# Optimization experiments

Hardware: AMD Instinct MI355X
Metric: run time of the kernel (lower is better)

## Reference

```python
import jax, jax.numpy as jnp
import numpy as np

N_HEADS = 16

def _rotate_half(t):
    # t: [B, H, T, hs]; split last dim in half, return cat(-x2, x1)
    hs = t.shape[-1]
    x1, x2 = t[..., : hs // 2], t[..., hs // 2 :]
    return jnp.concatenate((-x2, x1), axis=-1)

def _rope_pos(T, hs, dtype):
    inv_freq = 1.0 / (10000.0 ** (jnp.arange(0, hs, 2, dtype=jnp.float32) / hs))
    freqs = jnp.arange(T, dtype=jnp.float32)[:, None] * inv_freq[None, :]  # [T, hs/2]
    pos = jnp.concatenate((freqs, freqs), axis=-1)  # [T, hs]
    return pos

def setup_inputs() -> dict:
    key = jax.random.key(0)
    ks = jax.random.split(key, 5)
    d = 2048
    x = jax.random.normal(ks[0], (2, 2048, d), dtype=jnp.float32)
    W_attn = jax.random.normal(ks[1], (d, 3 * d), dtype=jnp.float32) * (1.0 / np.sqrt(d))
    b_attn = jax.random.normal(ks[2], (3 * d,), dtype=jnp.float32) * 0.02
    W_proj = jax.random.normal(ks[3], (d, d), dtype=jnp.float32) * (1.0 / np.sqrt(d))
    b_proj = jax.random.normal(ks[4], (d,), dtype=jnp.float32) * 0.02
    return {"x": x, "W_attn": W_attn, "b_attn": b_attn, "W_proj": W_proj, "b_proj": b_proj}

def reference(x, W_attn, b_attn, W_proj, b_proj):
    B, T, C = x.shape
    nh = N_HEADS
    hs = C // nh
    qkv = x @ W_attn + b_attn  # [B, T, 3C]
    q, k, v = jnp.split(qkv, 3, axis=-1)
    # [B, T, C] -> [B, nh, T, hs]
    def to_heads(t):
        return t.reshape(B, T, nh, hs).transpose(0, 2, 1, 3)
    q, k, v = to_heads(q), to_heads(k), to_heads(v)
    # RoPE
    pos = _rope_pos(T, hs, x.dtype)  # [T, hs]
    cos, sin = jnp.cos(pos).astype(x.dtype), jnp.sin(pos).astype(x.dtype)
    q = q * cos + _rotate_half(q) * sin
    k = k * cos + _rotate_half(k) * sin
    # causal SDPA
    scale = 1.0 / np.sqrt(hs)
    scores = jnp.einsum('bhqd,bhkd->bhqk', q, k) * scale  # [B, nh, T, T]
    causal = jnp.tril(jnp.ones((T, T), dtype=bool))
    scores = jnp.where(causal, scores, jnp.finfo(scores.dtype).min)
    att = jax.nn.softmax(scores, axis=-1)
    out = jnp.einsum('bhqk,bhkd->bhqd', att, v)  # [B, nh, T, hs]
    y = out.transpose(0, 2, 1, 3).reshape(B, T, C)
    return y @ W_proj + b_proj
```

## Files before the change

kernel.cpp:

```cpp
#include <hip/hip_runtime.h>
#include <stdint.h>

typedef unsigned short u16;
typedef __attribute__((ext_vector_type(8))) short short8;
typedef __attribute__((ext_vector_type(4))) float f32x4;
typedef __attribute__((ext_vector_type(4))) unsigned short u16x4;

#define DEV __device__ __forceinline__

DEV u16 f2bf(float f) {
  union { float f; unsigned u; } v; v.f = f;
  unsigned r = v.u + 0x7fffu + ((v.u >> 16) & 1u);
  return (u16)(r >> 16);
}
DEV float bf2f(u16 b) {
  union { unsigned u; float f; } v; v.u = ((unsigned)b) << 16;
  return v.f;
}
DEV void gload_lds16(const void* g, void* l) {
  __builtin_amdgcn_global_load_lds((const __attribute__((address_space(1))) void*)g,
                                   (__attribute__((address_space(3))) void*)l,
                                   16, 0, 0);
}
DEV void block_barrier() {
  asm volatile("" ::: "memory");
  __builtin_amdgcn_s_barrier();
  asm volatile("" ::: "memory");
}

__global__ void k_conv(const float* __restrict__ in, u16* __restrict__ out, int n4) {
  int i = blockIdx.x * blockDim.x + threadIdx.x;
  if (i >= n4) return;
  const f32x4 v = *(const f32x4*)(in + (size_t)i * 4);
  u16x4 o;
  o[0] = f2bf(v[0]); o[1] = f2bf(v[1]); o[2] = f2bf(v[2]); o[3] = f2bf(v[3]);
  *(u16x4*)(out + (size_t)i * 4) = o;
}

__global__ void k_tconv(const float* __restrict__ in, u16* __restrict__ out, int R, int C) {
  __shared__ float tile[32][33];
  int c0 = blockIdx.x * 32, r0 = blockIdx.y * 32;
  int tx = threadIdx.x, ty = threadIdx.y;
#pragma unroll
  for (int j = 0; j < 32; j += 8)
    tile[ty + j][tx] = in[(size_t)(r0 + ty + j) * C + (c0 + tx)];
  __syncthreads();
#pragma unroll
  for (int j = 0; j < 32; j += 8)
    out[(size_t)(c0 + ty + j) * R + (r0 + tx)] = f2bf(tile[tx][ty + j]);
}

__global__ void k_rope(const u16* __restrict__ qkv, u16* __restrict__ qh, u16* __restrict__ kh) {
  int m = blockIdx.x;
  int t = m & 2047, b = m >> 11;
  int tid = threadIdx.x;
  int h = blockIdx.y * 4 + (tid >> 6);
  int j = tid & 63;
  float inv = expf((float)j * -0.14391156831212787f);
  float ang = (float)t * inv;
  float s, c;
  sincosf(ang, &s, &c);
  size_t ibase = (size_t)m * 6144 + (size_t)h * 128;
  size_t obase = ((size_t)(b * 16 + h) * 2048 + t) * 128;
  float q1 = bf2f(qkv[ibase + j]),        q2 = bf2f(qkv[ibase + 64 + j]);
  qh[obase + j]      = f2bf(q1 * c - q2 * s);
  qh[obase + 64 + j] = f2bf(q2 * c + q1 * s);
  float k1 = bf2f(qkv[ibase + 2048 + j]), k2 = bf2f(qkv[ibase + 2048 + 64 + j]);
  kh[obase + j]      = f2bf(k1 * c - k2 * s);
  kh[obase + 64 + j] = f2bf(k2 * c + k1 * s);
}

__global__ void k_vtrans(const u16* __restrict__ qkv, u16* __restrict__ vt) {
  __shared__ u16 tile[32][33];
  int bh = blockIdx.z;
  int b = bh >> 4, h = bh & 15;
  int t0 = blockIdx.x * 32, d0 = blockIdx.y * 32;
  int tx = threadIdx.x, ty = threadIdx.y;
#pragma unroll
  for (int j = 0; j < 32; j += 8)
    tile[ty + j][tx] = qkv[(size_t)(b * 2048 + t0 + ty + j) * 6144 + 4096 + h * 128 + d0 + tx];
  __syncthreads();
#pragma unroll
  for (int j = 0; j < 32; j += 8)
    vt[((size_t)bh * 128 + d0 + ty + j) * 2048 + (t0 + tx)] = tile[tx][ty + j];
}

template <bool OUT_BF16, bool SPLITK>
__global__ __launch_bounds__(512, 2) void k_gemm3(const u16* __restrict__ A,
                                                  const u16* __restrict__ Bt,
                                                  const float* __restrict__ bias,
                                                  void* __restrict__ Cv,
                                                  int M, int N, int Kld, int nkt) {
  __shared__ __align__(16) short lA[2][256 * 64];
  __shared__ __align__(16) short lB[2][256 * 64];
  const int tid = threadIdx.x;
  const int wid = tid >> 6, lane = tid & 63;
  const int gx = gridDim.x;
  const int nwg = gx * gridDim.y;
  const int orig = blockIdx.y * gx + blockIdx.x;
  const int lg = (orig & 7) * (nwg >> 3) + (orig >> 3);
  const int bm = (lg % gx) * 256, bn = (lg / gx) * 256;
  const int wr = wid >> 2, wc = wid & 3;
  const int r = lane & 15, kq = lane >> 4, r7 = lane & 7;
  const int kz = SPLITK ? blockIdx.z * (nkt << 6) : 0;

  int aoff[4], boff[4], lbase[4];
#pragma unroll
  for (int j = 0; j < 4; ++j) {
    int c = j * 512 + wid * 64 + lane;
    int row = c >> 3, ch = c & 7;
    aoff[j] = (bm + row) * Kld + kz + (ch ^ (row & 7)) * 8;
    boff[j] = (bn + row) * Kld + kz + (ch ^ (row & 7)) * 8;
    lbase[j] = (j * 512 + wid * 64) * 16;
  }

#define STG_A(k0, buf, j) gload_lds16(A + aoff[j] + (k0), (char*)&lA[(buf)][0] + lbase[j])
#define STG_B(k0, buf, j) gload_lds16(Bt + boff[j] + (k0), (char*)&lB[(buf)][0] + lbase[j])
#define RD_A(AF, MH, KK)                                                        \
  _Pragma("unroll")                                                             \
  for (int m2 = 0; m2 < 4; ++m2)                                                \
    AF[m2] = *(const short8*)&As[(wr * 128 + (MH) * 64 + m2 * 16 + r) * 64      \
                                 + (((KK) * 4 + kq) ^ r7) * 8];
#define RD_B(KK)                                                                \
  _Pragma("unroll")                                                             \
  for (int nf = 0; nf < 4; ++nf)                                                \
    bfr[KK][nf] = *(const short8*)&Bs[(wc * 64 + nf * 16 + r) * 64              \
                                      + (((KK) * 4 + kq) ^ r7) * 8];
#define PH_MFMA(AF, MH, KK)                                                     \
  __builtin_amdgcn_s_setprio(1);                                                \
  _Pragma("unroll")                                                             \
  for (int m2 = 0; m2 < 4; ++m2)                                                \
    _Pragma("unroll")                                                           \
    for (int nf = 0; nf < 4; ++nf)                                              \
      acc[(MH) * 4 + m2][nf] = __builtin_amdgcn_mfma_f32_16x16x32_bf16(         \
          AF[m2], bfr[KK][nf], acc[(MH) * 4 + m2][nf], 0, 0, 0);                \
  __builtin_amdgcn_s_setprio(0);

  f32x4 acc[8][4];
  const f32x4 zero = {0.f, 0.f, 0.f, 0.f};
#pragma unroll
  for (int i = 0; i < 8; ++i)
#pragma unroll
    for (int j = 0; j < 4; ++j) acc[i][j] = zero;

  const int nt = nkt;

#pragma unroll
  for (int j = 0; j < 4; ++j) STG_A(0, 0, j);
#pragma unroll
  for (int j = 0; j < 4; ++j) STG_B(0, 0, j);
  if (nt > 1) {
#pragma unroll
    for (int j = 0; j < 4; ++j) STG_B(64, 1, j);
    asm volatile("s_waitcnt vmcnt(4)" ::: "memory");
  } else {
    asm volatile("s_waitcnt vmcnt(0)" ::: "memory");
  }
  block_barrier();

#pragma unroll 1
  for (int t = 0; t < nt; ++t) {
    const int cur = t & 1, nxt = cur ^ 1;
    const short* As = &lA[cur][0];
    const short* Bs = &lB[cur][0];
    const int kA = (t + 1) * 64, kB = (t + 2) * 64;
    const bool sA = (t + 1 < nt), sB = (t + 2 < nt);
    short8 bfr[2][4];
    short8 af[4];

    RD_B(0)
    RD_A(af, 0, 0)
    if (sA) { STG_A(kA, nxt, 0); STG_A(kA, nxt, 1); }
    block_barrier();
    PH_MFMA(af, 0, 0)
    block_barrier();

    RD_B(1)
    RD_A(af, 0, 1)
    if (sA) { STG_A(kA, nxt, 2); STG_A(kA, nxt, 3); }
    block_barrier();
    PH_MFMA(af, 0, 1)
    block_barrier();

    RD_A(af, 1, 0)
    if (sB) { STG_B(kB, cur, 0); STG_B(kB, cur, 1); }
    block_barrier();
    PH_MFMA(af, 1, 0)
    block_barrier();

    RD_A(af, 1, 1)
    if (sB) { STG_B(kB, cur, 2); STG_B(kB, cur, 3); }
    block_barrier();
    PH_MFMA(af, 1, 1)
    if (t + 1 < nt) {
      if (sB) asm volatile("s_waitcnt vmcnt(4)" ::: "memory");
      else    asm volatile("s_waitcnt vmcnt(0)" ::: "memory");
    }
    block_barrier();
  }
#undef STG_A
#undef STG_B
#undef RD_A
#undef RD_B
#undef PH_MFMA

#pragma unroll
  for (int mf = 0; mf < 8; ++mf)
#pragma unroll
    for (int nf = 0; nf < 4; ++nf) {
      int n = bn + wc * 64 + nf * 16 + r;
      float bv = SPLITK ? 0.f : bias[n];
#pragma unroll
      for (int i = 0; i < 4; ++i) {
        int m = bm + wr * 128 + mf * 16 + kq * 4 + i;
        float val = acc[mf][nf][i] + bv;
        if (SPLITK)
          ((float*)Cv)[(size_t)blockIdx.z * M * N + (size_t)m * N + n] = val;
        else if (OUT_BF16)
          ((u16*)Cv)[(size_t)m * N + n] = f2bf(val);
        else
          ((float*)Cv)[(size_t)m * N + n] = val;
      }
    }
}

__global__ void k_fadd(const float* __restrict__ p, const float* __restrict__ bias,
                       float* __restrict__ y, int n4) {
  const int half4 = 2097152;
  for (int i = blockIdx.x * blockDim.x + threadIdx.x; i < n4; i += gridDim.x * blockDim.x) {
    f32x4 a = *(const f32x4*)(p + (size_t)i * 4);
    f32x4 b = *(const f32x4*)(p + (size_t)(i + half4) * 4);
    f32x4 bv = *(const f32x4*)(bias + ((i & 511) << 2));
    f32x4 o = a + b + bv;
    *(f32x4*)(y + (size_t)i * 4) = o;
  }
}

__global__ __launch_bounds__(256) void k_attn(const u16* __restrict__ qh,
                                              const u16* __restrict__ kh,
                                              const u16* __restrict__ vt,
                                              u16* __restrict__ out) {
  __shared__ __align__(16) short lK[2][64 * 128];
  __shared__ __align__(16) short lV[2][128 * 64];
  __shared__ __align__(16) short lP[64 * 64];
  const int tid = threadIdx.x, wid = tid >> 6, lane = tid & 63;
  const int p = blockIdx.x, h = blockIdx.y, b = blockIdx.z;
  const size_t bh = (size_t)b * 16 + h;
  const u16* qb = qh + bh * 2048 * 128;
  const u16* kb = kh + bh * 2048 * 128;
  const u16* vb = vt + bh * 128 * 2048;
  const int r = lane & 15, kq = lane >> 4;
  const int r7 = r & 7;
  const int wrow = wid * 16;
  const float scale2 = 0.08838834764831845f * 1.4426950408889634f;

  int koff[4], voff[4];
#pragma unroll
  for (int i = 0; i < 4; ++i) {
    int ci = (wid * 4 + i) * 64 + lane;
    int krow = ci >> 4, kch = ci & 15;
    koff[i] = krow * 128 + ((kch ^ (krow & 7)) * 8);
    int vrow = ci >> 3, vch = ci & 7;
    voff[i] = vrow * 2048 + ((vch ^ (vrow & 7)) * 8);
  }

#pragma unroll 1
  for (int seg = 0; seg < 2; ++seg) {
    const int j = seg ? 31 - p : p;
    const int q0 = j * 64;
    const int nkt = j + 1;

    short8 qa[4];
#pragma unroll
    for (int kk = 0; kk < 4; ++kk)
      qa[kk] = *(const short8*)(qb + (size_t)(q0 + wrow + r) * 128 + kk * 32 + kq * 8);

    f32x4 O[8];
    const f32x4 zero = {0.f, 0.f, 0.f, 0.f};
#pragma unroll
    for (int nf = 0; nf < 8; ++nf) O[nf] = zero;
    float lp[4] = {0.f, 0.f, 0.f, 0.f};

#pragma unroll
    for (int i = 0; i < 4; ++i) {
      gload_lds16(kb + koff[i], (char*)&lK[0][0] + (wid * 4 + i) * 1024);
      gload_lds16(vb + voff[i], (char*)&lV[0][0] + (wid * 4 + i) * 1024);
    }

#pragma unroll 1
    for (int kt = 0; kt < nkt; ++kt) {
      const int cur = kt & 1;
      if (kt + 1 < nkt) {
        const size_t kbase = (size_t)(kt + 1) * 8192, vbase = (size_t)(kt + 1) * 64;
#pragma unroll
        for (int i = 0; i < 4; ++i) {
          gload_lds16(kb + kbase + koff[i], (char*)&lK[cur ^ 1][0] + (wid * 4 + i) * 1024);
          gload_lds16(vb + vbase + voff[i], (char*)&lV[cur ^ 1][0] + (wid * 4 + i) * 1024);
        }
        asm volatile("s_waitcnt vmcnt(8)" ::: "memory");
      } else {
        asm volatile("s_waitcnt vmcnt(0)" ::: "memory");
      }
      block_barrier();

      f32x4 S[4];
#pragma unroll
      for (int nf = 0; nf < 4; ++nf) S[nf] = zero;
#pragma unroll
      for (int kk = 0; kk < 4; ++kk) {
        short8 kf[4];
#pragma unroll
        for (int nf = 0; nf < 4; ++nf)
          kf[nf] = *(const short8*)&lK[cur][(nf * 16 + r) * 128 + ((kk * 4 + kq) ^ r7) * 8];
#pragma unroll
        for (int nf = 0; nf < 4; ++nf)
          S[nf] = __builtin_amdgcn_mfma_f32_16x16x32_bf16(qa[kk], kf[nf], S[nf], 0, 0, 0);
      }

      const bool diag = (kt == nkt - 1);
#pragma unroll
      for (int nf = 0; nf < 4; ++nf)
#pragma unroll
        for (int i = 0; i < 4; ++i) {
          float pv = exp2f(S[nf][i] * scale2);
          if (diag) {
            int kg = kt * 64 + nf * 16 + r;
            int qg = q0 + wrow + kq * 4 + i;
            pv = (kg > qg) ? 0.f : pv;
          }
          lp[i] += pv;
          int row = wrow + kq * 4 + i;
          int cl = (nf * 2 + (r >> 3)) ^ ((kq * 4 + i) & 7);
          lP[row * 64 + cl * 8 + r7] = (short)f2bf(pv);
        }

#pragma unroll
      for (int kk = 0; kk < 2; ++kk) {
        short8 pa = *(const short8*)&lP[(wrow + r) * 64 + ((kk * 4 + kq) ^ r7) * 8];
#pragma unroll
        for (int nf = 0; nf < 8; ++nf) {
          short8 vf = *(const short8*)&lV[cur][(nf * 16 + r) * 64 + ((kk * 4 + kq) ^ r7) * 8];
          O[nf] = __builtin_amdgcn_mfma_f32_16x16x32_bf16(pa, vf, O[nf], 0, 0, 0);
        }
      }
      asm volatile("s_waitcnt lgkmcnt(0)" ::: "memory");
      block_barrier();
    }

    float inv[4];
#pragma unroll
    for (int i = 0; i < 4; ++i) {
      float v = lp[i];
      v += __shfl_xor(v, 1);
      v += __shfl_xor(v, 2);
      v += __shfl_xor(v, 4);
      v += __shfl_xor(v, 8);
      inv[i] = 1.f / v;
    }
#pragma unroll
    for (int nf = 0; nf < 8; ++nf)
#pragma unroll
      for (int i = 0; i < 4; ++i) {
        int qg = q0 + wrow + kq * 4 + i;
        out[(size_t)(b * 2048 + qg) * 2048 + h * 128 + nf * 16 + r] = f2bf(O[nf][i] * inv[i]);
      }
  }
}

extern "C" void kernel_launch(void* const* d_in, const int* in_sizes, int n_in,
                              void* d_out, int out_size, void* d_ws, size_t ws_size,
                              hipStream_t stream) {
  const float* x      = (const float*)d_in[0];
  const float* W_attn = (const float*)d_in[1];
  const float* b_attn = (const float*)d_in[2];
  const float* W_proj = (const float*)d_in[3];
  const float* b_proj = (const float*)d_in[4];
  float* y = (float*)d_out;

  u16* xb     = (u16*)d_ws;
  u16* wqkvT  = xb     + (size_t)4096 * 2048;
  u16* wprojT = wqkvT  + (size_t)6144 * 2048;
  u16* qkv    = wprojT + (size_t)2048 * 2048;
  u16* qh     = qkv    + (size_t)4096 * 6144;
  u16* kh     = qh     + (size_t)4096 * 2048;
  u16* vt     = kh     + (size_t)4096 * 2048;
  u16* attout = vt     + (size_t)4096 * 2048;
  if (ws_size < (size_t)83886080 * 2) return;

  float* pproj = (float*)qkv;

  k_conv<<<8192, 256, 0, stream>>>(x, xb, 2097152);
  k_tconv<<<dim3(192, 64), dim3(32, 8), 0, stream>>>(W_attn, wqkvT, 2048, 6144);
  k_tconv<<<dim3(64, 64), dim3(32, 8), 0, stream>>>(W_proj, wprojT, 2048, 2048);
  k_gemm3<true, false><<<dim3(16, 24), 512, 0, stream>>>(xb, wqkvT, b_attn, qkv, 4096, 6144, 2048, 32);
  k_rope<<<dim3(4096, 4), 256, 0, stream>>>(qkv, qh, kh);
  k_vtrans<<<dim3(64, 4, 32), dim3(32, 8), 0, stream>>>(qkv, vt);
  k_attn<<<dim3(16, 16, 2), 256, 0, stream>>>(qh, kh, vt, attout);
  k_gemm3<false, true><<<dim3(16, 8, 2), 512, 0, stream>>>(attout, wprojT, b_proj, pproj, 4096, 2048, 2048, 16);
  k_fadd<<<2048, 256, 0, stream>>>(pproj, b_proj, y, 2097152);
}
```

Baseline: 314.7 us.

## Fuse RoPE and V transpose into QKV GEMM epilogue

Adds a dedicated QKV GEMM whose epilogue applies bias and RoPE and writes Q and K directly in head-major layout. It also writes V transposed, so the separate rope and vtrans kernels and the qkv intermediate are gone. Partner half-dimension values for the rotation are exchanged through LDS, and the angle is advanced with a recurrence after one sincos per fragment. This removes two launches and the round trip of the qkv buffer through global memory. In exchange the epilogue has scattered stores and extra barriers, and the sincos recurrence adds a little numeric drift.

```diff
diff --git a/kernel.cpp b/kernel.cpp
--- a/kernel.cpp
+++ b/kernel.cpp
@@ -50,47 +50,13 @@
     out[(size_t)(c0 + ty + j) * R + (r0 + tx)] = f2bf(tile[tx][ty + j]);
 }
 
-__global__ void k_rope(const u16* __restrict__ qkv, u16* __restrict__ qh, u16* __restrict__ kh) {
-  int m = blockIdx.x;
-  int t = m & 2047, b = m >> 11;
-  int tid = threadIdx.x;
-  int h = blockIdx.y * 4 + (tid >> 6);
-  int j = tid & 63;
-  float inv = expf((float)j * -0.14391156831212787f);
-  float ang = (float)t * inv;
-  float s, c;
-  sincosf(ang, &s, &c);
-  size_t ibase = (size_t)m * 6144 + (size_t)h * 128;
-  size_t obase = ((size_t)(b * 16 + h) * 2048 + t) * 128;
-  float q1 = bf2f(qkv[ibase + j]),        q2 = bf2f(qkv[ibase + 64 + j]);
-  qh[obase + j]      = f2bf(q1 * c - q2 * s);
-  qh[obase + 64 + j] = f2bf(q2 * c + q1 * s);
-  float k1 = bf2f(qkv[ibase + 2048 + j]), k2 = bf2f(qkv[ibase + 2048 + 64 + j]);
-  kh[obase + j]      = f2bf(k1 * c - k2 * s);
-  kh[obase + 64 + j] = f2bf(k2 * c + k1 * s);
-}
-
-__global__ void k_vtrans(const u16* __restrict__ qkv, u16* __restrict__ vt) {
-  __shared__ u16 tile[32][33];
-  int bh = blockIdx.z;
-  int b = bh >> 4, h = bh & 15;
-  int t0 = blockIdx.x * 32, d0 = blockIdx.y * 32;
-  int tx = threadIdx.x, ty = threadIdx.y;
-#pragma unroll
-  for (int j = 0; j < 32; j += 8)
-    tile[ty + j][tx] = qkv[(size_t)(b * 2048 + t0 + ty + j) * 6144 + 4096 + h * 128 + d0 + tx];
-  __syncthreads();
-#pragma unroll
-  for (int j = 0; j < 32; j += 8)
-    vt[((size_t)bh * 128 + d0 + ty + j) * 2048 + (t0 + tx)] = tile[tx][ty + j];
-}
-
-template <bool OUT_BF16, bool SPLITK>
-__global__ __launch_bounds__(512, 2) void k_gemm3(const u16* __restrict__ A,
-                                                  const u16* __restrict__ Bt,
-                                                  const float* __restrict__ bias,
-                                                  void* __restrict__ Cv,
-                                                  int M, int N, int Kld, int nkt) {
+__global__ __launch_bounds__(512, 2) void k_gemmqkv(const u16* __restrict__ A,
+                                                    const u16* __restrict__ Bt,
+                                                    const float* __restrict__ bias,
+                                                    u16* __restrict__ qh,
+                                                    u16* __restrict__ kh,
+                                                    u16* __restrict__ vt) {
+  const int Kld = 2048, nt = 32;
   __shared__ __align__(16) short lA[2][256 * 64];
   __shared__ __align__(16) short lB[2][256 * 64];
   const int tid = threadIdx.x;
@@ -102,15 +68,14 @@
   const int bm = (lg % gx) * 256, bn = (lg / gx) * 256;
   const int wr = wid >> 2, wc = wid & 3;
   const int r = lane & 15, kq = lane >> 4, r7 = lane & 7;
-  const int kz = SPLITK ? blockIdx.z * (nkt << 6) : 0;
 
   int aoff[4], boff[4], lbase[4];
 #pragma unroll
   for (int j = 0; j < 4; ++j) {
     int c = j * 512 + wid * 64 + lane;
     int row = c >> 3, ch = c & 7;
-    aoff[j] = (bm + row) * Kld + kz + (ch ^ (row & 7)) * 8;
-    boff[j] = (bn + row) * Kld + kz + (ch ^ (row & 7)) * 8;
+    aoff[j] = (bm + row) * Kld + (ch ^ (row & 7)) * 8;
+    boff[j] = (bn + row) * Kld + (ch ^ (row & 7)) * 8;
     lbase[j] = (j * 512 + wid * 64) * 16;
   }
 
@@ -143,6 +108,185 @@
 #pragma unroll
     for (int j = 0; j < 4; ++j) acc[i][j] = zero;
 
+#pragma unroll
+  for (int j = 0; j < 4; ++j) STG_A(0, 0, j);
+#pragma unroll
+  for (int j = 0; j < 4; ++j) STG_B(0, 0, j);
+#pragma unroll
+  for (int j = 0; j < 4; ++j) STG_B(64, 1, j);
+  asm volatile("s_waitcnt vmcnt(4)" ::: "memory");
+  block_barrier();
+
+#pragma unroll 1
+  for (int t = 0; t < nt; ++t) {
+    const int cur = t & 1, nxt = cur ^ 1;
+    const short* As = &lA[cur][0];
+    const short* Bs = &lB[cur][0];
+    const int kA = (t + 1) * 64, kB = (t + 2) * 64;
+    const bool sA = (t + 1 < nt), sB = (t + 2 < nt);
+    short8 bfr[2][4];
+    short8 af[4];
+
+    RD_B(0)
+    RD_A(af, 0, 0)
+    if (sA) { STG_A(kA, nxt, 0); STG_A(kA, nxt, 1); }
+    block_barrier();
+    PH_MFMA(af, 0, 0)
+    block_barrier();
+
+    RD_B(1)
+    RD_A(af, 0, 1)
+    if (sA) { STG_A(kA, nxt, 2); STG_A(kA, nxt, 3); }
+    block_barrier();
+    PH_MFMA(af, 0, 1)
+    block_barrier();
+
+    RD_A(af, 1, 0)
+    if (sB) { STG_B(kB, cur, 0); STG_B(kB, cur, 1); }
+    block_barrier();
+    PH_MFMA(af, 1, 0)
+    block_barrier();
+
+    RD_A(af, 1, 1)
+    if (sB) { STG_B(kB, cur, 2); STG_B(kB, cur, 3); }
+    block_barrier();
+    PH_MFMA(af, 1, 1)
+    if (t + 1 < nt) {
+      if (sB) asm volatile("s_waitcnt vmcnt(4)" ::: "memory");
+      else    asm volatile("s_waitcnt vmcnt(0)" ::: "memory");
+    }
+    block_barrier();
+  }
+#undef STG_A
+#undef STG_B
+#undef RD_A
+#undef RD_B
+#undef PH_MFMA
+
+  const int by = lg / gx;
+  const int part = by >> 3;
+  const int b_ = bm >> 11;
+  const int tb = (bm & 2047) + wr * 128;
+
+  if (part == 2) {
+#pragma unroll
+    for (int nf = 0; nf < 4; ++nf) {
+      int n = bn + wc * 64 + nf * 16 + r;
+      int nl = n & 2047;
+      int hh = nl >> 7, d = nl & 127;
+      float bv = bias[n];
+      u16* vrow = vt + ((size_t)(b_ * 16 + hh) * 128 + d) * 2048;
+#pragma unroll
+      for (int mf = 0; mf < 8; ++mf) {
+        int t = tb + mf * 16 + kq * 4;
+        u16x4 o;
+#pragma unroll
+        for (int i = 0; i < 4; ++i) o[i] = f2bf(acc[mf][nf][i] + bv);
+        *(u16x4*)(vrow + t) = o;
+      }
+    }
+  } else {
+    u16* dst = part ? kh : qh;
+    float* fb = (float*)&lA[0][0];
+    const int hi = wc & 1;
+    int nn[4]; float bvn[4], invf[4], c1v[4], s1v[4];
+    size_t drow[4];
+#pragma unroll
+    for (int nf = 0; nf < 4; ++nf) {
+      nn[nf] = bn + wc * 64 + nf * 16 + r;
+      bvn[nf] = bias[nn[nf]];
+      invf[nf] = exp2f((float)(nf * 16 + r) * -0.20762050593045077f);
+      sincosf(invf[nf], &s1v[nf], &c1v[nf]);
+      int nl = nn[nf] & 2047;
+      drow[nf] = (size_t)(b_ * 16 + (nl >> 7)) * 2048 * 128 + (nl & 127);
+    }
+#pragma unroll 1
+    for (int mf = 0; mf < 8; ++mf) {
+#pragma unroll
+      for (int nf = 0; nf < 4; ++nf)
+#pragma unroll
+        for (int i = 0; i < 4; ++i)
+          fb[((wid * 4 + nf) * 4 + i) * 64 + r * 4 + kq] = acc[mf][nf][i] + bvn[nf];
+      block_barrier();
+#pragma unroll
+      for (int nf = 0; nf < 4; ++nf) {
+        int t0 = tb + mf * 16 + kq * 4;
+        float cs, sn;
+        sincosf((float)t0 * invf[nf], &sn, &cs);
+#pragma unroll
+        for (int i = 0; i < 4; ++i) {
+          float v0 = acc[mf][nf][i] + bvn[nf];
+          float pv = fb[(((wid ^ 1) * 4 + nf) * 4 + i) * 64 + r * 4 + kq];
+          float vr = hi ? (v0 * cs + pv * sn) : (v0 * cs - pv * sn);
+          dst[drow[nf] + (size_t)(t0 + i) * 128] = f2bf(vr);
+          float cn = cs * c1v[nf] - sn * s1v[nf];
+          sn = sn * c1v[nf] + cs * s1v[nf];
+          cs = cn;
+        }
+      }
+      block_barrier();
+    }
+  }
+}
+
+template <bool OUT_BF16, bool SPLITK>
+__global__ __launch_bounds__(512, 2) void k_gemm3(const u16* __restrict__ A,
+                                                  const u16* __restrict__ Bt,
+                                                  const float* __restrict__ bias,
+                                                  void* __restrict__ Cv,
+                                                  int M, int N, int Kld, int nkt) {
+  __shared__ __align__(16) short lA[2][256 * 64];
+  __shared__ __align__(16) short lB[2][256 * 64];
+  const int tid = threadIdx.x;
+  const int wid = tid >> 6, lane = tid & 63;
+  const int gx = gridDim.x;
+  const int nwg = gx * gridDim.y;
+  const int orig = blockIdx.y * gx + blockIdx.x;
+  const int lg = (orig & 7) * (nwg >> 3) + (orig >> 3);
+  const int bm = (lg % gx) * 256, bn = (lg / gx) * 256;
+  const int wr = wid >> 2, wc = wid & 3;
+  const int r = lane & 15, kq = lane >> 4, r7 = lane & 7;
+  const int kz = SPLITK ? blockIdx.z * (nkt << 6) : 0;
+
+  int aoff[4], boff[4], lbase[4];
+#pragma unroll
+  for (int j = 0; j < 4; ++j) {
+    int c = j * 512 + wid * 64 + lane;
+    int row = c >> 3, ch = c & 7;
+    aoff[j] = (bm + row) * Kld + kz + (ch ^ (row & 7)) * 8;
+    boff[j] = (bn + row) * Kld + kz + (ch ^ (row & 7)) * 8;
+    lbase[j] = (j * 512 + wid * 64) * 16;
+  }
+
+#define STG_A(k0, buf, j) gload_lds16(A + aoff[j] + (k0), (char*)&lA[(buf)][0] + lbase[j])
+#define STG_B(k0, buf, j) gload_lds16(Bt + boff[j] + (k0), (char*)&lB[(buf)][0] + lbase[j])
+#define RD_A(AF, MH, KK)                                                        \
+  _Pragma("unroll")                                                             \
+  for (int m2 = 0; m2 < 4; ++m2)                                                \
+    AF[m2] = *(const short8*)&As[(wr * 128 + (MH) * 64 + m2 * 16 + r) * 64      \
+                                 + (((KK) * 4 + kq) ^ r7) * 8];
+#define RD_B(KK)                                                                \
+  _Pragma("unroll")                                                             \
+  for (int nf = 0; nf < 4; ++nf)                                                \
+    bfr[KK][nf] = *(const short8*)&Bs[(wc * 64 + nf * 16 + r) * 64              \
+                                      + (((KK) * 4 + kq) ^ r7) * 8];
+#define PH_MFMA(AF, MH, KK)                                                     \
+  __builtin_amdgcn_s_setprio(1);                                                \
+  _Pragma("unroll")                                                             \
+  for (int m2 = 0; m2 < 4; ++m2)                                                \
+    _Pragma("unroll")                                                           \
+    for (int nf = 0; nf < 4; ++nf)                                              \
+      acc[(MH) * 4 + m2][nf] = __builtin_amdgcn_mfma_f32_16x16x32_bf16(         \
+          AF[m2], bfr[KK][nf], acc[(MH) * 4 + m2][nf], 0, 0, 0);                \
+  __builtin_amdgcn_s_setprio(0);
+
+  f32x4 acc[8][4];
+  const f32x4 zero = {0.f, 0.f, 0.f, 0.f};
+#pragma unroll
+  for (int i = 0; i < 8; ++i)
+#pragma unroll
+    for (int j = 0; j < 4; ++j) acc[i][j] = zero;
+
   const int nt = nkt;
 
 #pragma unroll
@@ -392,9 +536,7 @@
   k_conv<<<8192, 256, 0, stream>>>(x, xb, 2097152);
   k_tconv<<<dim3(192, 64), dim3(32, 8), 0, stream>>>(W_attn, wqkvT, 2048, 6144);
   k_tconv<<<dim3(64, 64), dim3(32, 8), 0, stream>>>(W_proj, wprojT, 2048, 2048);
-  k_gemm3<true, false><<<dim3(16, 24), 512, 0, stream>>>(xb, wqkvT, b_attn, qkv, 4096, 6144, 2048, 32);
-  k_rope<<<dim3(4096, 4), 256, 0, stream>>>(qkv, qh, kh);
-  k_vtrans<<<dim3(64, 4, 32), dim3(32, 8), 0, stream>>>(qkv, vt);
+  k_gemmqkv<<<dim3(16, 24), 512, 0, stream>>>(xb, wqkvT, b_attn, qh, kh, vt);
   k_attn<<<dim3(16, 16, 2), 256, 0, stream>>>(qh, kh, vt, attout);
   k_gemm3<false, true><<<dim3(16, 8, 2), 512, 0, stream>>>(attout, wprojT, b_proj, pproj, 4096, 2048, 2048, 16);
   k_fadd<<<2048, 256, 0, stream>>>(pproj, b_proj, y, 2097152);
```

Result: slower. 374.6 us (+19.1%).
